# Kernel optimization log

Measured on AMD Instinct MI355X. Metric: run time of the kernel, lower is better.

## Reference

```python
import jax, jax.numpy as jnp
import numpy as np

HID = 2048      # hidden_size
NH = 32         # num_heads
QLR = 1536      # q_lora_rank
KVLR = 512      # kv_lora_rank
DR = 64         # qk_rope_head_dim
DN = 128        # qk_nope_head_dim
DV = 128        # v_head_dim
DQK = DN + DR   # 192
EPS = 1e-6
ROPE_BASE = 10000.0


def rms_norm(x, w):
    return x * jax.lax.rsqrt(jnp.mean(x * x, axis=-1, keepdims=True) + EPS) * w


def apply_rope(x, pos):
    # x: [B, S, H, d] (non-interleaved / rotate-half convention), pos: [S]
    d = x.shape[-1]
    inv_freq = 1.0 / (ROPE_BASE ** (jnp.arange(0, d, 2, dtype=jnp.float32) / d))
    freqs = pos[:, None].astype(jnp.float32) * inv_freq      # [S, d/2]
    cos = jnp.cos(freqs)[None, :, None, :]                   # [1, S, 1, d/2]
    sin = jnp.sin(freqs)[None, :, None, :]
    x1, x2 = x[..., : d // 2], x[..., d // 2:]
    return jnp.concatenate([x1 * cos - x2 * sin, x1 * sin + x2 * cos], axis=-1)


def setup_inputs() -> dict:
    key = jax.random.key(0)
    ks = jax.random.split(key, 8)
    s = 0.02
    return {
        "hidden_states": jax.random.normal(ks[0], (1, 2048, HID), jnp.float32),
        "q_a_w":    jax.random.normal(ks[1], (HID, QLR), jnp.float32) * s,
        "q_a_ln_w": jnp.ones((QLR,), jnp.float32),
        "q_b_w":    jax.random.normal(ks[2], (QLR, NH * DQK), jnp.float32) * s,
        "kv_a_w":   jax.random.normal(ks[3], (HID, KVLR + DR), jnp.float32) * s,
        "kv_a_ln_w": jnp.ones((KVLR,), jnp.float32),
        "kv_b_w":   jax.random.normal(ks[4], (KVLR, NH * (DN + DV)), jnp.float32) * s,
        "o_w":      jax.random.normal(ks[5], (NH * DV, HID), jnp.float32) * s,
    }


def reference(hidden_states, q_a_w, q_a_ln_w, q_b_w, kv_a_w, kv_a_ln_w, kv_b_w, o_w):
    B, S, _ = hidden_states.shape
    # low-rank Q: down-proj -> RMSNorm -> up-proj
    q = rms_norm(hidden_states @ q_a_w, q_a_ln_w) @ q_b_w       # [B,S,NH*DQK]
    q = q.reshape(B, S, NH, DQK)
    q_pass, q_rot = q[..., :DN], q[..., DN:]
    # compressed KV + shared rope key
    ckv = hidden_states @ kv_a_w                                # [B,S,KVLR+DR]
    c_kv, k_rot = ckv[..., :KVLR], ckv[..., KVLR:]
    kv = rms_norm(c_kv, kv_a_ln_w) @ kv_b_w                     # [B,S,NH*(DN+DV)]
    kv = kv.reshape(B, S, NH, DN + DV)
    k_pass, v = kv[..., :DN], kv[..., DN:]
    # RoPE
    pos = jnp.arange(S)
    q_rot = apply_rope(q_rot, pos)                              # [B,S,NH,DR]
    k_rot = apply_rope(k_rot[:, :, None, :], pos)[:, :, 0, :]   # [B,S,DR] (shared head)
    # causal attention, scale = qk_head_dim**-0.5
    scale = DQK ** -0.5
    scores = (jnp.einsum('bqhd,bkhd->bhqk', q_pass, k_pass)
              + jnp.einsum('bqhd,bkd->bhqk', q_rot, k_rot)) * scale
    causal = jnp.tril(jnp.ones((S, S), dtype=bool))
    scores = jnp.where(causal[None, None], scores, jnp.finfo(scores.dtype).min)
    p = jax.nn.softmax(scores, axis=-1)
    out = jnp.einsum('bhqk,bkhd->bqhd', p, v).reshape(B, S, NH * DV)
    return out @ o_w
```

## Files before the change

kernel.cpp:

```cpp
#include <hip/hip_runtime.h>


typedef __bf16 bf16x8 __attribute__((ext_vector_type(8)));
typedef float  f32x4  __attribute__((ext_vector_type(4)));
typedef unsigned u32x4 __attribute__((ext_vector_type(4)));

#define GLOAD16(g, l)                                                          \
  __builtin_amdgcn_global_load_lds(                                            \
      (const __attribute__((address_space(1))) unsigned int*)(g),              \
      (__attribute__((address_space(3))) unsigned int*)(l), 16, 0, 0)

__device__ __forceinline__ unsigned short f2b(float f) {
  unsigned u = __builtin_bit_cast(unsigned, f);
  u += 0x7fffu + ((u >> 16) & 1u);
  return (unsigned short)(u >> 16);
}

__device__ __forceinline__ unsigned cvtpk(float lo, float hi) {
  unsigned r;
  asm("v_cvt_pk_bf16_f32 %0, %1, %2" : "=v"(r) : "v"(lo), "v"(hi));
  return r;
}

__device__ __forceinline__ void tc_body(const float* __restrict__ src,
                                        unsigned short* __restrict__ dst,
                                        int R, int C, int bx, int by,
                                        int tx, int ty) {
  __shared__ float t[32][33];
  int r0 = bx * 32, c0 = by * 32;
#pragma unroll
  for (int j = 0; j < 4; j++) {
    int c = c0 + tx;
    t[ty + j * 8][tx] = (c < C) ? src[(size_t)(r0 + ty + j * 8) * C + c] : 0.f;
  }
  __syncthreads();
#pragma unroll
  for (int j = 0; j < 4; j++)
    dst[(size_t)(c0 + ty + j * 8) * R + r0 + tx] = f2b(t[tx][ty + j * 8]);
}

__global__ __launch_bounds__(256) void prep(
    const float* __restrict__ hs, unsigned short* __restrict__ hs_b,
    const float* __restrict__ qaw, const float* __restrict__ kvaw,
    unsigned short* __restrict__ wcat,
    const float* __restrict__ qbw, unsigned short* __restrict__ qbT,
    const float* __restrict__ kvbw, unsigned short* __restrict__ kvbT,
    const float* __restrict__ ow, unsigned short* __restrict__ owT) {
  int b = blockIdx.x;
// ... 146 lines not shown
    for (int n = 0; n < 4; n++) {
      int row = wn * 64 + n * 16 + lr;
      b[n] = *(const bf16x8*)(Bs + row * 32 + ((lh ^ swzr) * 8));
    }
#pragma unroll
    for (int m = 0; m < 4; m++)
#pragma unroll
      for (int n = 0; n < 4; n++)
        acc[m][n] = __builtin_amdgcn_mfma_f32_16x16x32_bf16(a[m], b[n], acc[m][n], 0, 0, 0);
    __syncthreads();
  }
#pragma unroll
  for (int m = 0; m < 4; m++)
#pragma unroll
    for (int n = 0; n < 4; n++)
#pragma unroll
      for (int r = 0; r < 4; r++) {
        int row = m0 + wm * 64 + m * 16 + lh * 4 + r;
        int col = n0 + wn * 64 + n * 16 + lr;
        C[(size_t)row * N + col] = acc[m][n][r];
      }
}

__global__ __launch_bounds__(512) void gemm256m(
    const unsigned short* __restrict__ Aq, const unsigned short* __restrict__ Bq,
    unsigned short* __restrict__ Qb,
    const unsigned short* __restrict__ Akv, const unsigned short* __restrict__ Bkv,
    unsigned short* __restrict__ Kb, unsigned short* __restrict__ Vt) {
  __shared__ unsigned short lds[2][2][16384];
  const int tid = threadIdx.x;
  const int w = tid >> 6, lane = tid & 63;
  const int lr = lane & 15, lh = lane >> 4;
  const int wr = w >> 2, wc = w & 3;
  const int blk = blockIdx.x;
  const bool isq = blk < 192;
  const int bx = isq ? (blk % 24) : ((blk - 192) & 31);
  const int by = isq ? (blk / 24) : ((blk - 192) >> 5);
  const int K  = isq ? 1536 : 512;
  const unsigned short* A  = isq ? Aq : Akv;
  const unsigned short* Bt = isq ? Bq : Bkv;
  const int m0 = by * 256, n0 = bx * 256;

  int soff[2];
#pragma unroll
  for (int j = 0; j < 2; j++) {
    int c = j * 512 + tid;
    int row = c >> 3, p = c & 7;
    soff[j] = row * K + (p ^ (row & 7)) * 8;
  }
  const unsigned short* Abase = A + (size_t)m0 * K;
  const unsigned short* Bbase = Bt + (size_t)n0 * K;
  const int rswz = lr & 7;

#define STAGEOP(op, Base, kt, buf)                                             \
  {                                                                            \
    _Pragma("unroll") for (int hh = 0; hh < 2; hh++)                           \
    _Pragma("unroll") for (int j = 0; j < 2; j++)                              \
      GLOAD16(Base + (size_t)(hh * 128) * K + soff[j] + (kt) * 64,             \
              &lds[buf][op][(hh * 1024 + j * 512 + w * 64) * 8]);              \
  }
#define READA(mh, buf)                                                         \
  {                                                                            \
    _Pragma("unroll") for (int mi = 0; mi < 4; mi++)                           \
    _Pragma("unroll") for (int ks = 0; ks < 2; ks++)                           \
      af[mi][ks] = *(const bf16x8*)&lds[buf][0][                               \
          (wr * 128 + ((mh) * 4 + mi) * 16 + lr) * 64 +                        \
          (((ks * 4 + lh) ^ rswz) * 8)];                                       \
// ... 137 lines not shown
  const int lin = blockIdx.x;
  const int sid = (lin & 7) * 32 + (lin >> 3);
  const int s = sid >> 6, rem = sid & 63;
  const int m0 = (rem >> 3) * 256, n0 = (rem & 7) * 256;
  const int Kst = 4096;
  const int koff = s * 1024;

  int soff[2];
#pragma unroll
  for (int j = 0; j < 2; j++) {
    int c = j * 512 + tid;
    int row = c >> 3, p = c & 7;
    soff[j] = row * Kst + (p ^ (row & 7)) * 8;
  }
  const unsigned short* Abase = A + (size_t)m0 * Kst + koff;
  const unsigned short* Bbase = Bt + (size_t)n0 * Kst + koff;
  const int rswz = lr & 7;

#define STAGEOP(op, Base, kt, buf)                                             \
  {                                                                            \
    _Pragma("unroll") for (int hh = 0; hh < 2; hh++)                           \
    _Pragma("unroll") for (int j = 0; j < 2; j++)                              \
      GLOAD16(Base + (size_t)(hh * 128) * Kst + soff[j] + (kt) * 64,           \
              &lds[buf][op][(hh * 1024 + j * 512 + w * 64) * 8]);              \
  }
#define READA(mh, buf)                                                         \
  {                                                                            \
    _Pragma("unroll") for (int mi = 0; mi < 4; mi++)                           \
    _Pragma("unroll") for (int ks = 0; ks < 2; ks++)                           \
      af[mi][ks] = *(const bf16x8*)&lds[buf][0][                               \
          (wr * 128 + ((mh) * 4 + mi) * 16 + lr) * 64 +                        \
          (((ks * 4 + lh) ^ rswz) * 8)];                                       \
  }
#define READB(n, buf)                                                          \
  {                                                                            \
    _Pragma("unroll") for (int ks = 0; ks < 2; ks++)                           \
      bfr[n][ks] = *(const bf16x8*)&lds[buf][1][                               \
          (wc * 64 + (n) * 16 + lr) * 64 + (((ks * 4 + lh) ^ rswz) * 8)];      \
  }
#define MFMAQ(mh, nh)                                                          \
  {                                                                            \
    __builtin_amdgcn_s_setprio(1);                                             \
    _Pragma("unroll") for (int mi = 0; mi < 4; mi++)                           \
    _Pragma("unroll") for (int ni = 0; ni < 2; ni++)                           \
    _Pragma("unroll") for (int ks = 0; ks < 2; ks++)                           \
      acc[(mh) * 4 + mi][(nh) * 2 + ni] =                                      \
          __builtin_amdgcn_mfma_f32_16x16x32_bf16(                             \
              af[mi][ks], bfr[(nh) * 2 + ni][ks],                              \
              acc[(mh) * 4 + mi][(nh) * 2 + ni], 0, 0, 0);                     \
    __builtin_amdgcn_s_setprio(0);                                             \
  }

  f32x4 acc[8][4];
  const f32x4 z = {0.f, 0.f, 0.f, 0.f};
#pragma unroll
  for (int i = 0; i < 8; i++)
#pragma unroll
    for (int j = 0; j < 4; j++) acc[i][j] = z;

  STAGEOP(0, Abase, 0, 0);
  STAGEOP(1, Bbase, 0, 0);
  asm volatile("s_waitcnt vmcnt(0)" ::: "memory");
  __builtin_amdgcn_s_barrier();

  const int KT = 16;
  for (int kt = 0; kt < KT; ++kt) {
    const int buf = kt & 1;
// ... 9 lines not shown
    if (more) STAGEOP(1, Bbase, kt + 1, buf ^ 1);
    __builtin_amdgcn_s_barrier();
    MFMAQ(0, 1);
    __builtin_amdgcn_s_barrier();
    READA(1, buf);
    __builtin_amdgcn_s_barrier();
    MFMAQ(1, 1);
    __builtin_amdgcn_s_barrier();
    MFMAQ(1, 0);
    if (more) asm volatile("s_waitcnt vmcnt(0)" ::: "memory");
    __builtin_amdgcn_s_barrier();
  }
#undef STAGEOP
#undef READA
#undef READB
#undef MFMAQ

  float* C = Cp + (size_t)s * 2048 * 2048;
#pragma unroll
  for (int m = 0; m < 8; m++)
#pragma unroll
    for (int n = 0; n < 4; n++)
#pragma unroll
      for (int r = 0; r < 4; r++) {
        int row = m0 + wr * 128 + m * 16 + lh * 4 + r;
        int col = n0 + wc * 64 + n * 16 + lr;
        C[(size_t)row * 2048 + col] = acc[m][n][r];
      }
}

__global__ __launch_bounds__(512) void attn(const unsigned short* __restrict__ Qb,
                                            const unsigned short* __restrict__ Kb,
                                            const unsigned short* __restrict__ Vt,
                                            unsigned short* __restrict__ O) {
  __shared__ unsigned short Kl[2][12288];
  __shared__ unsigned short Vl[2][8192];
  const int tid = threadIdx.x;
  const int w = tid >> 6, lane = tid & 63;
  const int lr = lane & 15, lh = lane >> 4;
  const int b = blockIdx.x;
  const int x = b & 7, k = b >> 3;
  const int h = x + 8 * (k >> 4);
  const int ii = k & 15;
  int qi = (ii & 1) ? (15 - 2 * (ii >> 1)) : (2 * (ii >> 1));
  if (k & 32) qi = 15 - qi;
  const int q0 = qi * 128;
  const int qw = q0 + w * 16;
  const int qv = qw + lr;

  bf16x8 qf[6];
#pragma unroll
  for (int c = 0; c < 6; c++)
    qf[c] = *(const bf16x8*)(Qb + (size_t)(qw + lr) * 6144 + h * 192 + c * 32 + lh * 8);

  const unsigned short* Kbase = Kb + h * 192;
  const unsigned short* Vbase = Vt + (size_t)h * 128 * 2048;
  size_t ka[3];
#pragma unroll
  for (int j = 0; j < 3; j++) {
    int c = tid + j * 512;
    int r = c / 24, p = c - r * 24;
    ka[j] = (size_t)r * 6144 + (p ^ (r & 7)) * 8;
  }
  size_t va[2];
#pragma unroll
  for (int j = 0; j < 2; j++) {
    int c = tid + j * 512;
    int d = c >> 3, p = c & 7;
    va[j] = (size_t)d * 2048 + (p ^ (d & 7)) * 8;
  }

#define STAGE(T0, B)                                                           \
  {                                                                            \
    _Pragma("unroll") for (int j = 0; j < 3; j++)                              \
        GLOAD16(Kbase + (size_t)(T0) * 6144 + ka[j], &Kl[B][(tid + j * 512) * 8]); \
    _Pragma("unroll") for (int j = 0; j < 2; j++)                              \
        GLOAD16(Vbase + va[j] + (T0), &Vl[B][(tid + j * 512) * 8]);            \
  }

  f32x4 acc[8];
  const f32x4 z = {0.f, 0.f, 0.f, 0.f};
#pragma unroll
  for (int n = 0; n < 8; n++) acc[n] = z;
  float mrow = -1e30f, lrow = 0.f;
  const int swz = (lr & 7) * 8;
  const int cv0 = ((lh ^ (lr & 7)) * 8);
  const int cv1 = (((4 + lh) ^ (lr & 7)) * 8);
  const int sA = lr + 32 * (lh & 1), sB = sA + 16;

  const int nt = (q0 + 128) >> 6;
  STAGE(0, 0);
  __syncthreads();
  for (int it = 0; it < nt; ++it) {
    const int t0 = it << 6;
    const int cur = it & 1;
    if (it + 1 < nt) STAGE(t0 + 64, cur ^ 1);
    if (t0 <= qw + 15) {
      f32x4 s0 = z, s1 = z, s2 = z, s3 = z;
      __builtin_amdgcn_s_setprio(1);
#pragma unroll
      for (int c = 0; c < 6; c++) {
        int col = ((c * 4 + lh) * 8) ^ swz;
        bf16x8 k0 = *(const bf16x8*)(&Kl[cur][(lr)      * 192 + col]);
        bf16x8 k1 = *(const bf16x8*)(&Kl[cur][(16 + lr) * 192 + col]);
        bf16x8 k2 = *(const bf16x8*)(&Kl[cur][(32 + lr) * 192 + col]);
        bf16x8 k3 = *(const bf16x8*)(&Kl[cur][(48 + lr) * 192 + col]);
        s0 = __builtin_amdgcn_mfma_f32_16x16x32_bf16(k0, qf[c], s0, 0, 0, 0);
        s1 = __builtin_amdgcn_mfma_f32_16x16x32_bf16(k1, qf[c], s1, 0, 0, 0);
        s2 = __builtin_amdgcn_mfma_f32_16x16x32_bf16(k2, qf[c], s2, 0, 0, 0);
        s3 = __builtin_amdgcn_mfma_f32_16x16x32_bf16(k3, qf[c], s3, 0, 0, 0);
      }
      __builtin_amdgcn_s_setprio(0);
      const int tb = t0 + lh * 4;
      if (t0 + 63 > qw) {
#pragma unroll
        for (int r = 0; r < 4; r++) {
          s0[r] = (tb + r > qv)      ? -1e30f : s0[r];
          s1[r] = (tb + 16 + r > qv) ? -1e30f : s1[r];
          s2[r] = (tb + 32 + r > qv) ? -1e30f : s2[r];
          s3[r] = (tb + 48 + r > qv) ? -1e30f : s3[r];
        }
      }
      float mx = -1e30f;
#pragma unroll
      for (int r = 0; r < 4; r++)
        mx = fmaxf(mx, fmaxf(fmaxf(s0[r], s1[r]), fmaxf(s2[r], s3[r])));
      mx = fmaxf(mx, __shfl_xor(mx, 16, 64));
      mx = fmaxf(mx, __shfl_xor(mx, 32, 64));
      float ro = 1.f;
      bool resc = (mx - mrow) > 11.5f;
      if (resc) { ro = exp2f(mrow - mx); mrow = mx; }
      float p0[4], p1[4], p2[4], p3[4], ls = 0.f;
#pragma unroll
      for (int r = 0; r < 4; r++) {
        p0[r] = exp2f(s0[r] - mrow);
        p1[r] = exp2f(s1[r] - mrow);
        p2[r] = exp2f(s2[r] - mrow);
        p3[r] = exp2f(s3[r] - mrow);
        ls += (p0[r] + p1[r]) + (p2[r] + p3[r]);
      }
      lrow = lrow * ro + ls;
      if (__any(resc)) {
        float rs[4];
#pragma unroll
        for (int r = 0; r < 4; r++) rs[r] = __shfl(ro, lh * 4 + r, 16);
#pragma unroll
        for (int n = 0; n < 8; n++)
#pragma unroll
          for (int r = 0; r < 4; r++) acc[n][r] *= rs[r];
      }
      unsigned k0p = cvtpk(p0[0], p0[1]), k1p = cvtpk(p0[2], p0[3]);
      unsigned k2p = cvtpk(p1[0], p1[1]), k3p = cvtpk(p1[2], p1[3]);
      unsigned k4p = cvtpk(p2[0], p2[1]), k5p = cvtpk(p2[2], p2[3]);
      unsigned k6p = cvtpk(p3[0], p3[1]), k7p = cvtpk(p3[2], p3[3]);
      u32x4 w0, w1;
      {
        unsigned A0 = __shfl(k0p, sA, 64), A1 = __shfl(k1p, sA, 64);
        unsigned B0 = __shfl(k0p, sB, 64), B1 = __shfl(k1p, sB, 64);
        unsigned C0 = __shfl(k2p, sA, 64), C1 = __shfl(k3p, sA, 64);
        unsigned D0 = __shfl(k2p, sB, 64), D1 = __shfl(k3p, sB, 64);
        w0[0] = (lh < 2) ? A0 : C0;
        w0[1] = (lh < 2) ? A1 : C1;
        w0[2] = (lh < 2) ? B0 : D0;
        w0[3] = (lh < 2) ? B1 : D1;
      }
      {
        unsigned A0 = __shfl(k4p, sA, 64), A1 = __shfl(k5p, sA, 64);
        unsigned B0 = __shfl(k4p, sB, 64), B1 = __shfl(k5p, sB, 64);
        unsigned C0 = __shfl(k6p, sA, 64), C1 = __shfl(k7p, sA, 64);
        unsigned D0 = __shfl(k6p, sB, 64), D1 = __shfl(k7p, sB, 64);
        w1[0] = (lh < 2) ? A0 : C0;
        w1[1] = (lh < 2) ? A1 : C1;
        w1[2] = (lh < 2) ? B0 : D0;
        w1[3] = (lh < 2) ? B1 : D1;
      }
      bf16x8 pa0 = __builtin_bit_cast(bf16x8, w0);
      bf16x8 pa1 = __builtin_bit_cast(bf16x8, w1);
      __builtin_amdgcn_s_setprio(1);
#pragma unroll
      for (int n = 0; n < 8; n++) {
        bf16x8 vb0 = *(const bf16x8*)(&Vl[cur][(n * 16 + lr) * 64 + cv0]);
        bf16x8 vb1 = *(const bf16x8*)(&Vl[cur][(n * 16 + lr) * 64 + cv1]);
        acc[n] = __builtin_amdgcn_mfma_f32_16x16x32_bf16(pa0, vb0, acc[n], 0, 0, 0);
        acc[n] = __builtin_amdgcn_mfma_f32_16x16x32_bf16(pa1, vb1, acc[n], 0, 0, 0);
      }
      __builtin_amdgcn_s_setprio(0);
    }
    __syncthreads();
  }
#undef STAGE
  lrow += __shfl_xor(lrow, 16, 64);
  lrow += __shfl_xor(lrow, 32, 64);
  float invL = 1.f / lrow;
  float inv[4];
#pragma unroll
  for (int r = 0; r < 4; r++) inv[r] = __shfl(invL, lh * 4 + r, 16);
#pragma unroll
  for (int n = 0; n < 8; n++)
#pragma unroll
    for (int r = 0; r < 4; r++) {
      int q = qw + lh * 4 + r;
      O[(size_t)q * 4096 + h * 128 + n * 16 + lr] = f2b(acc[n][r] * inv[r]);
    }
}

extern "C" void kernel_launch(void* const* d_in, const int* in_sizes, int n_in,
                              void* d_out, int out_size, void* d_ws, size_t ws_size,
                              hipStream_t stream) {
  const float* hs      = (const float*)d_in[0];
  const float* q_a_w   = (const float*)d_in[1];
  const float* q_a_ln  = (const float*)d_in[2];
  const float* q_b_w   = (const float*)d_in[3];
  const float* kv_a_w  = (const float*)d_in[4];
  const float* kv_a_ln = (const float*)d_in[5];
  const float* kv_b_w  = (const float*)d_in[6];
  const float* o_w     = (const float*)d_in[7];
  float* out = (float*)d_out;

  char* ws = (char*)d_ws;
  size_t off = 0;
  auto alloc = [&](size_t bytes) {
    void* p = ws + off;
    off += (bytes + 255) & ~(size_t)255;
    return p;
  };
  unsigned short* wcat    = (unsigned short*)alloc(2176UL * 2048 * 2);
  unsigned short* q_b_wT  = (unsigned short*)alloc(6144UL * 1536 * 2);
  unsigned short* kv_b_wT = (unsigned short*)alloc(8192UL * 512 * 2);
  unsigned short* o_wT    = (unsigned short*)alloc(2048UL * 4096 * 2);
  unsigned short* hs_b    = (unsigned short*)alloc(2048UL * 2048 * 2);
  unsigned short* q_a_n   = (unsigned short*)alloc(2048UL * 1536 * 2);
  unsigned short* Qb      = (unsigned short*)alloc(2048UL * 6144 * 2);
  unsigned short* ckv_n   = (unsigned short*)alloc(2048UL * 512 * 2);
  unsigned short* Kb      = (unsigned short*)alloc(2048UL * 6144 * 2);
  unsigned short* Vt      = (unsigned short*)alloc(32UL * 128 * 2048 * 2);
  float*          OutP    = (float*)Qb;
  char* big = (char*)alloc(2UL * 2048 * 2176 * 4);
  float*          Craw0    = (float*)big;
  float*          Craw1    = (float*)(big + 2048UL * 2176 * 4);
  unsigned short* attn_out = (unsigned short*)big;
  (void)ws_size; (void)in_sizes; (void)n_in; (void)out_size;

  dim3 b256(256), b512(512);
  prep<<<29952, b256, 0, stream>>>(hs, hs_b, q_a_w, kv_a_w, wcat,
                                   q_b_w, q_b_wT, kv_b_w, kv_b_wT, o_w, o_wT);
  gemm_bt<<<544, b256, 0, stream>>>(hs_b, wcat, Craw0, 2048, 2176, 2048, 17, 272, 2);
  rms2<<<4096, b256, 0, stream>>>(Craw0, Craw1, q_a_ln, kv_a_ln, q_a_n, ckv_n, Kb);
  gemm256m<<<448, b512, 0, stream>>>(q_a_n, q_b_wT, Qb, ckv_n, kv_b_wT, Kb, Vt);
  attn<<<512, b512, 0, stream>>>(Qb, Kb, Vt, attn_out);
  gemm256_op<<<256, b512, 0, stream>>>(attn_out, o_wT, OutP);
  addout<<<4096, b256, 0, stream>>>((const float4*)OutP, (float4*)out);
}
```

Before: 287.2 us.

## Split attention KV range by parity into two partials and add combine kernel

Attention blocks now each handle a pair of complementary query tiles (qi and 15-qi) and only the even or odd 32-key tiles, writing unnormalized-style partial outputs plus (max, sum) stats. A new combine kernel merges the two parity partials with log-sum-exp weights. The aim is to balance causal work evenly across blocks and to use smaller LDS tiles for better occupancy. The cost is an extra kernel launch, extra partial-output memory traffic and bf16 rounding of partials. The GEMM block index is also remapped for a different workgroup-to-CU distribution.

Measured after the change: 313.3 us. 1.09x slower.

```diff
diff --git a/kernel.cpp b/kernel.cpp
--- a/kernel.cpp
+++ b/kernel.cpp
@@ -14,6 +14,10 @@
   unsigned u = __builtin_bit_cast(unsigned, f);
   u += 0x7fffu + ((u >> 16) & 1u);
   return (unsigned short)(u >> 16);
+}
+
+__device__ __forceinline__ float b2f(unsigned short u) {
+  return __builtin_bit_cast(float, (unsigned)u << 16);
 }
 
 __device__ __forceinline__ unsigned cvtpk(float lo, float hi) {
@@ -226,7 +230,8 @@
   const int w = tid >> 6, lane = tid & 63;
   const int lr = lane & 15, lh = lane >> 4;
   const int wr = w >> 2, wc = w & 3;
-  const int blk = blockIdx.x;
+  const int lin = blockIdx.x;
+  const int blk = (lin & 7) * 56 + (lin >> 3);
   const bool isq = blk < 192;
   const int bx = isq ? (blk % 24) : ((blk - 192) & 31);
   const int by = isq ? (blk / 24) : ((blk - 192) >> 5);
@@ -506,176 +511,194 @@
 __global__ __launch_bounds__(512) void attn(const unsigned short* __restrict__ Qb,
                                             const unsigned short* __restrict__ Kb,
                                             const unsigned short* __restrict__ Vt,
-                                            unsigned short* __restrict__ O) {
-  __shared__ unsigned short Kl[2][12288];
-  __shared__ unsigned short Vl[2][8192];
+                                            unsigned short* __restrict__ Po,
+                                            float2* __restrict__ Ml) {
+  __shared__ unsigned short Kl[2][6144];
+  __shared__ unsigned short Vl[2][4096];
   const int tid = threadIdx.x;
   const int w = tid >> 6, lane = tid & 63;
   const int lr = lane & 15, lh = lane >> 4;
   const int b = blockIdx.x;
-  const int x = b & 7, k = b >> 3;
-  const int h = x + 8 * (k >> 4);
-  const int ii = k & 15;
-  int qi = (ii & 1) ? (15 - 2 * (ii >> 1)) : (2 * (ii >> 1));
-  if (k & 32) qi = 15 - qi;
-  const int q0 = qi * 128;
-  const int qw = q0 + w * 16;
-  const int qv = qw + lr;
-
-  bf16x8 qf[6];
-#pragma unroll
-  for (int c = 0; c < 6; c++)
-    qf[c] = *(const bf16x8*)(Qb + (size_t)(qw + lr) * 6144 + h * 192 + c * 32 + lh * 8);
+  const int x = b & 7, r_ = b >> 3;
+  const int h = x + 8 * (r_ & 3);
+  const int p = r_ >> 2;
+  const int a = p >> 1, par = p & 1;
 
   const unsigned short* Kbase = Kb + h * 192;
   const unsigned short* Vbase = Vt + (size_t)h * 128 * 2048;
-  size_t ka[3];
-#pragma unroll
-  for (int j = 0; j < 3; j++) {
-    int c = tid + j * 512;
-    int r = c / 24, p = c - r * 24;
-    ka[j] = (size_t)r * 6144 + (p ^ (r & 7)) * 8;
-  }
-  size_t va[2];
-#pragma unroll
-  for (int j = 0; j < 2; j++) {
-    int c = tid + j * 512;
-    int d = c >> 3, p = c & 7;
-    va[j] = (size_t)d * 2048 + (p ^ (d & 7)) * 8;
+  size_t kga0, kga1 = 0;
+  {
+    int c = w * 64 + lane;
+    int rr = c / 24, pp = c - rr * 24;
+    kga0 = (size_t)rr * 6144 + (pp ^ (rr & 7)) * 8;
+  }
+  if (w < 4) {
+    int c = 512 + w * 64 + lane;
+    int rr = c / 24, pp = c - rr * 24;
+    kga1 = (size_t)rr * 6144 + (pp ^ (rr & 7)) * 8;
+  }
+  size_t vga;
+  {
+    int c = w * 64 + lane;
+    int d = c >> 2, pp = c & 3;
+    vga = (size_t)d * 2048 + (pp ^ ((d >> 1) & 3)) * 8;
   }
 
 #define STAGE(T0, B)                                                           \
   {                                                                            \
-    _Pragma("unroll") for (int j = 0; j < 3; j++)                              \
-        GLOAD16(Kbase + (size_t)(T0) * 6144 + ka[j], &Kl[B][(tid + j * 512) * 8]); \
-    _Pragma("unroll") for (int j = 0; j < 2; j++)                              \
-        GLOAD16(Vbase + va[j] + (T0), &Vl[B][(tid + j * 512) * 8]);            \
-  }
-
-  f32x4 acc[8];
+    GLOAD16(Kbase + (size_t)(T0) * 6144 + kga0, &Kl[B][w * 512]);              \
+    if (w < 4)                                                                 \
+      GLOAD16(Kbase + (size_t)(T0) * 6144 + kga1, &Kl[B][4096 + w * 512]);     \
+    GLOAD16(Vbase + vga + (T0), &Vl[B][w * 512]);                              \
+  }
+
+  const int swz = (lr & 7) * 8;
+  const int vsw = (lh ^ ((lr >> 1) & 3)) * 8;
+  const int sA = lr + 32 * (lh & 1), sB = sA + 16;
   const f32x4 z = {0.f, 0.f, 0.f, 0.f};
-#pragma unroll
-  for (int n = 0; n < 8; n++) acc[n] = z;
-  float mrow = -1e30f, lrow = 0.f;
-  const int swz = (lr & 7) * 8;
-  const int cv0 = ((lh ^ (lr & 7)) * 8);
-  const int cv1 = (((4 + lh) ^ (lr & 7)) * 8);
-  const int sA = lr + 32 * (lh & 1), sB = sA + 16;
-
-  const int nt = (q0 + 128) >> 6;
-  STAGE(0, 0);
-  __syncthreads();
-  for (int it = 0; it < nt; ++it) {
-    const int t0 = it << 6;
-    const int cur = it & 1;
-    if (it + 1 < nt) STAGE(t0 + 64, cur ^ 1);
-    if (t0 <= qw + 15) {
-      f32x4 s0 = z, s1 = z, s2 = z, s3 = z;
-      __builtin_amdgcn_s_setprio(1);
-#pragma unroll
-      for (int c = 0; c < 6; c++) {
-        int col = ((c * 4 + lh) * 8) ^ swz;
-        bf16x8 k0 = *(const bf16x8*)(&Kl[cur][(lr)      * 192 + col]);
-        bf16x8 k1 = *(const bf16x8*)(&Kl[cur][(16 + lr) * 192 + col]);
-        bf16x8 k2 = *(const bf16x8*)(&Kl[cur][(32 + lr) * 192 + col]);
-        bf16x8 k3 = *(const bf16x8*)(&Kl[cur][(48 + lr) * 192 + col]);
-        s0 = __builtin_amdgcn_mfma_f32_16x16x32_bf16(k0, qf[c], s0, 0, 0, 0);
-        s1 = __builtin_amdgcn_mfma_f32_16x16x32_bf16(k1, qf[c], s1, 0, 0, 0);
-        s2 = __builtin_amdgcn_mfma_f32_16x16x32_bf16(k2, qf[c], s2, 0, 0, 0);
-        s3 = __builtin_amdgcn_mfma_f32_16x16x32_bf16(k3, qf[c], s3, 0, 0, 0);
+
+  for (int job = 0; job < 2; ++job) {
+    const int qi = job ? (15 - a) : a;
+    const int q0 = qi << 7;
+    const int qw = q0 + w * 16;
+    const int qv = qw + lr;
+    const int cnt = 2 * (qi + 1);
+
+    bf16x8 qf[6];
+#pragma unroll
+    for (int cc = 0; cc < 6; cc++)
+      qf[cc] = *(const bf16x8*)(Qb + (size_t)(qw + lr) * 6144 + h * 192 + cc * 32 + lh * 8);
+
+    f32x4 acc[8];
+#pragma unroll
+    for (int n = 0; n < 8; n++) acc[n] = z;
+    float mrow = -1e30f, lrow = 0.f;
+
+    STAGE((size_t)(par) << 5, 0);
+    __syncthreads();
+    for (int k = 0; k < cnt; ++k) {
+      const int t0 = (par + 2 * k) << 5;
+      const int cur = k & 1;
+      if (k + 1 < cnt) STAGE((size_t)(par + 2 * (k + 1)) << 5, cur ^ 1);
+      if (t0 <= qw + 15) {
+        f32x4 s0 = z, s1 = z;
+        __builtin_amdgcn_s_setprio(1);
+#pragma unroll
+        for (int cc = 0; cc < 6; cc++) {
+          int col = ((cc * 4 + lh) * 8) ^ swz;
+          bf16x8 k0 = *(const bf16x8*)(&Kl[cur][lr * 192 + col]);
+          bf16x8 k1 = *(const bf16x8*)(&Kl[cur][(16 + lr) * 192 + col]);
+          s0 = __builtin_amdgcn_mfma_f32_16x16x32_bf16(k0, qf[cc], s0, 0, 0, 0);
+          s1 = __builtin_amdgcn_mfma_f32_16x16x32_bf16(k1, qf[cc], s1, 0, 0, 0);
+        }
+        __builtin_amdgcn_s_setprio(0);
+        const int tb = t0 + lh * 4;
+        if (t0 + 31 > qw) {
+#pragma unroll
+          for (int r = 0; r < 4; r++) {
+            s0[r] = (tb + r > qv)      ? -1e30f : s0[r];
+            s1[r] = (tb + 16 + r > qv) ? -1e30f : s1[r];
+          }
+        }
+        float mx = -1e30f;
+#pragma unroll
+        for (int r = 0; r < 4; r++)
+          mx = fmaxf(mx, fmaxf(s0[r], s1[r]));
+        mx = fmaxf(mx, __shfl_xor(mx, 16, 64));
+        mx = fmaxf(mx, __shfl_xor(mx, 32, 64));
+        float ro = 1.f;
+        bool resc = (mx - mrow) > 11.5f;
+        if (resc) { ro = exp2f(mrow - mx); mrow = mx; }
+        float p0[4], p1[4], ls = 0.f;
+#pragma unroll
+        for (int r = 0; r < 4; r++) {
+          p0[r] = exp2f(s0[r] - mrow);
+          p1[r] = exp2f(s1[r] - mrow);
+          ls += p0[r] + p1[r];
+        }
+        lrow = lrow * ro + ls;
+        if (__any(resc)) {
+          float rs[4];
+#pragma unroll
+          for (int r = 0; r < 4; r++) rs[r] = __shfl(ro, lh * 4 + r, 16);
+#pragma unroll
+          for (int n = 0; n < 8; n++)
+#pragma unroll
+            for (int r = 0; r < 4; r++) acc[n][r] *= rs[r];
+        }
+        unsigned pk0 = cvtpk(p0[0], p0[1]), pk1 = cvtpk(p0[2], p0[3]);
+        unsigned pk2 = cvtpk(p1[0], p1[1]), pk3 = cvtpk(p1[2], p1[3]);
+        unsigned A0 = __shfl(pk0, sA, 64), A1 = __shfl(pk1, sA, 64);
+        unsigned B0 = __shfl(pk0, sB, 64), B1 = __shfl(pk1, sB, 64);
+        unsigned C0 = __shfl(pk2, sA, 64), C1 = __shfl(pk3, sA, 64);
+        unsigned D0 = __shfl(pk2, sB, 64), D1 = __shfl(pk3, sB, 64);
+        u32x4 pw;
+        pw[0] = (lh < 2) ? A0 : C0;
+        pw[1] = (lh < 2) ? A1 : C1;
+        pw[2] = (lh < 2) ? B0 : D0;
+        pw[3] = (lh < 2) ? B1 : D1;
+        bf16x8 pa = __builtin_bit_cast(bf16x8, pw);
+        __builtin_amdgcn_s_setprio(1);
+#pragma unroll
+        for (int n = 0; n < 8; n++) {
+          bf16x8 vb = *(const bf16x8*)(&Vl[cur][(n * 16 + lr) * 32 + vsw]);
+          acc[n] = __builtin_amdgcn_mfma_f32_16x16x32_bf16(pa, vb, acc[n], 0, 0, 0);
+        }
+        __builtin_amdgcn_s_setprio(0);
       }
-      __builtin_amdgcn_s_setprio(0);
-      const int tb = t0 + lh * 4;
-      if (t0 + 63 > qw) {
-#pragma unroll
-        for (int r = 0; r < 4; r++) {
-          s0[r] = (tb + r > qv)      ? -1e30f : s0[r];
-          s1[r] = (tb + 16 + r > qv) ? -1e30f : s1[r];
-          s2[r] = (tb + 32 + r > qv) ? -1e30f : s2[r];
-          s3[r] = (tb + 48 + r > qv) ? -1e30f : s3[r];
-        }
+      __syncthreads();
+    }
+    lrow += __shfl_xor(lrow, 16, 64);
+    lrow += __shfl_xor(lrow, 32, 64);
+    float invL = (lrow > 0.f) ? (1.f / lrow) : 0.f;
+    float inv[4];
+#pragma unroll
+    for (int r = 0; r < 4; r++) inv[r] = __shfl(invL, lh * 4 + r, 16);
+    unsigned short* Pob = Po + (size_t)par * 8388608;
+#pragma unroll
+    for (int n = 0; n < 8; n++)
+#pragma unroll
+      for (int r = 0; r < 4; r++) {
+        int q = qw + lh * 4 + r;
+        Pob[(size_t)q * 4096 + h * 128 + n * 16 + lr] = f2b(acc[n][r] * inv[r]);
       }
-      float mx = -1e30f;
-#pragma unroll
-      for (int r = 0; r < 4; r++)
-        mx = fmaxf(mx, fmaxf(fmaxf(s0[r], s1[r]), fmaxf(s2[r], s3[r])));
-      mx = fmaxf(mx, __shfl_xor(mx, 16, 64));
-      mx = fmaxf(mx, __shfl_xor(mx, 32, 64));
-      float ro = 1.f;
-      bool resc = (mx - mrow) > 11.5f;
-      if (resc) { ro = exp2f(mrow - mx); mrow = mx; }
-      float p0[4], p1[4], p2[4], p3[4], ls = 0.f;
-#pragma unroll
-      for (int r = 0; r < 4; r++) {
-        p0[r] = exp2f(s0[r] - mrow);
-        p1[r] = exp2f(s1[r] - mrow);
-        p2[r] = exp2f(s2[r] - mrow);
-        p3[r] = exp2f(s3[r] - mrow);
-        ls += (p0[r] + p1[r]) + (p2[r] + p3[r]);
-      }
-      lrow = lrow * ro + ls;
-      if (__any(resc)) {
-        float rs[4];
-#pragma unroll
-        for (int r = 0; r < 4; r++) rs[r] = __shfl(ro, lh * 4 + r, 16);
-#pragma unroll
-        for (int n = 0; n < 8; n++)
-#pragma unroll
-          for (int r = 0; r < 4; r++) acc[n][r] *= rs[r];
-      }
-      unsigned k0p = cvtpk(p0[0], p0[1]), k1p = cvtpk(p0[2], p0[3]);
-      unsigned k2p = cvtpk(p1[0], p1[1]), k3p = cvtpk(p1[2], p1[3]);
-      unsigned k4p = cvtpk(p2[0], p2[1]), k5p = cvtpk(p2[2], p2[3]);
-      unsigned k6p = cvtpk(p3[0], p3[1]), k7p = cvtpk(p3[2], p3[3]);
-      u32x4 w0, w1;
-      {
-        unsigned A0 = __shfl(k0p, sA, 64), A1 = __shfl(k1p, sA, 64);
-        unsigned B0 = __shfl(k0p, sB, 64), B1 = __shfl(k1p, sB, 64);
-        unsigned C0 = __shfl(k2p, sA, 64), C1 = __shfl(k3p, sA, 64);
-        unsigned D0 = __shfl(k2p, sB, 64), D1 = __shfl(k3p, sB, 64);
-        w0[0] = (lh < 2) ? A0 : C0;
-        w0[1] = (lh < 2) ? A1 : C1;
-        w0[2] = (lh < 2) ? B0 : D0;
-        w0[3] = (lh < 2) ? B1 : D1;
-      }
-      {
-        unsigned A0 = __shfl(k4p, sA, 64), A1 = __shfl(k5p, sA, 64);
-        unsigned B0 = __shfl(k4p, sB, 64), B1 = __shfl(k5p, sB, 64);
-        unsigned C0 = __shfl(k6p, sA, 64), C1 = __shfl(k7p, sA, 64);
-        unsigned D0 = __shfl(k6p, sB, 64), D1 = __shfl(k7p, sB, 64);
-        w1[0] = (lh < 2) ? A0 : C0;
-        w1[1] = (lh < 2) ? A1 : C1;
-        w1[2] = (lh < 2) ? B0 : D0;
-        w1[3] = (lh < 2) ? B1 : D1;
-      }
-      bf16x8 pa0 = __builtin_bit_cast(bf16x8, w0);
-      bf16x8 pa1 = __builtin_bit_cast(bf16x8, w1);
-      __builtin_amdgcn_s_setprio(1);
-#pragma unroll
-      for (int n = 0; n < 8; n++) {
-        bf16x8 vb0 = *(const bf16x8*)(&Vl[cur][(n * 16 + lr) * 64 + cv0]);
-        bf16x8 vb1 = *(const bf16x8*)(&Vl[cur][(n * 16 + lr) * 64 + cv1]);
-        acc[n] = __builtin_amdgcn_mfma_f32_16x16x32_bf16(pa0, vb0, acc[n], 0, 0, 0);
-        acc[n] = __builtin_amdgcn_mfma_f32_16x16x32_bf16(pa1, vb1, acc[n], 0, 0, 0);
-      }
-      __builtin_amdgcn_s_setprio(0);
-    }
-    __syncthreads();
+    if (lh == 0) {
+      float2 ml; ml.x = mrow; ml.y = lrow;
+      Ml[(size_t)par * 65536 + h * 2048 + qw + lr] = ml;
+    }
   }
 #undef STAGE
-  lrow += __shfl_xor(lrow, 16, 64);
-  lrow += __shfl_xor(lrow, 32, 64);
-  float invL = 1.f / lrow;
-  float inv[4];
-#pragma unroll
-  for (int r = 0; r < 4; r++) inv[r] = __shfl(invL, lh * 4 + r, 16);
-#pragma unroll
-  for (int n = 0; n < 8; n++)
-#pragma unroll
-    for (int r = 0; r < 4; r++) {
-      int q = qw + lh * 4 + r;
-      O[(size_t)q * 4096 + h * 128 + n * 16 + lr] = f2b(acc[n][r] * inv[r]);
-    }
+}
+
+__global__ __launch_bounds__(256) void combine(const unsigned short* __restrict__ Po,
+                                               const float2* __restrict__ Ml,
+                                               unsigned short* __restrict__ Out) {
+  int gid = blockIdx.x * 256 + threadIdx.x;
+  int row = gid >> 4, seg = gid & 15;
+  int q = row >> 5, h = row & 31;
+  float2 ml0 = Ml[h * 2048 + q];
+  float2 ml1 = Ml[65536 + h * 2048 + q];
+  float M = fmaxf(ml0.x, ml1.x);
+  float w0 = ml0.y * exp2f(ml0.x - M);
+  float w1 = ml1.y * exp2f(ml1.x - M);
+  float inv = 1.f / (w0 + w1);
+  w0 *= inv; w1 *= inv;
+  size_t off = (size_t)q * 4096 + h * 128 + seg * 8;
+  ushort4 a0 = *(const ushort4*)(Po + off);
+  ushort4 a1 = *(const ushort4*)(Po + off + 4);
+  ushort4 b0 = *(const ushort4*)(Po + 8388608 + off);
+  ushort4 b1 = *(const ushort4*)(Po + 8388608 + off + 4);
+  ushort4 o0, o1;
+  o0.x = f2b(w0 * b2f(a0.x) + w1 * b2f(b0.x));
+  o0.y = f2b(w0 * b2f(a0.y) + w1 * b2f(b0.y));
+  o0.z = f2b(w0 * b2f(a0.z) + w1 * b2f(b0.z));
+  o0.w = f2b(w0 * b2f(a0.w) + w1 * b2f(b0.w));
+  o1.x = f2b(w0 * b2f(a1.x) + w1 * b2f(b1.x));
+  o1.y = f2b(w0 * b2f(a1.y) + w1 * b2f(b1.y));
+  o1.z = f2b(w0 * b2f(a1.z) + w1 * b2f(b1.z));
+  o1.w = f2b(w0 * b2f(a1.w) + w1 * b2f(b1.w));
+  *(ushort4*)(Out + off) = o0;
+  *(ushort4*)(Out + off + 4) = o1;
 }
 
 extern "C" void kernel_launch(void* const* d_in, const int* in_sizes, int n_in,
@@ -712,7 +735,9 @@
   char* big = (char*)alloc(2UL * 2048 * 2176 * 4);
   float*          Craw0    = (float*)big;
   float*          Craw1    = (float*)(big + 2048UL * 2176 * 4);
-  unsigned short* attn_out = (unsigned short*)big;
+  unsigned short* Po       = (unsigned short*)big;
+  float2*         Ml       = (float2*)alloc(2UL * 32 * 2048 * 8);
+  unsigned short* attn_out = (unsigned short*)alloc(2048UL * 4096 * 2);
   (void)ws_size; (void)in_sizes; (void)n_in; (void)out_size;
 
   dim3 b256(256), b512(512);
@@ -721,7 +746,8 @@
   gemm_bt<<<544, b256, 0, stream>>>(hs_b, wcat, Craw0, 2048, 2176, 2048, 17, 272, 2);
   rms2<<<4096, b256, 0, stream>>>(Craw0, Craw1, q_a_ln, kv_a_ln, q_a_n, ckv_n, Kb);
   gemm256m<<<448, b512, 0, stream>>>(q_a_n, q_b_wT, Qb, ckv_n, kv_b_wT, Kb, Vt);
-  attn<<<512, b512, 0, stream>>>(Qb, Kb, Vt, attn_out);
+  attn<<<512, b512, 0, stream>>>(Qb, Kb, Vt, Po, Ml);
+  combine<<<4096, b256, 0, stream>>>(Po, Ml, attn_out);
   gemm256_op<<<256, b512, 0, stream>>>(attn_out, o_wT, OutP);
   addout<<<4096, b256, 0, stream>>>((const float4*)OutP, (float4*)out);
 }
```

## Split attention KV range by tile parity and merge partials in combine kernel

Applied to the files above, without the earlier changes.

Each attention block now handles one head, one KV parity (even or odd 64-key tiles), and two paired query tiles (a and 15-a). This balances causal work across blocks, which previously varied with query-tile position. Each half writes normalized bf16 partial outputs plus the row max and sum. A new combine kernel merges the two partials with log-sum-exp weights. The cost is an extra launch, extra global traffic for the partials, and extra bf16 rounding of the intermediate results.

After: 299.7 us. +4.3%, slower.

```diff
diff --git a/kernel.cpp b/kernel.cpp
--- a/kernel.cpp
+++ b/kernel.cpp
@@ -14,6 +14,10 @@
   unsigned u = __builtin_bit_cast(unsigned, f);
   u += 0x7fffu + ((u >> 16) & 1u);
   return (unsigned short)(u >> 16);
+}
+
+__device__ __forceinline__ float b2f(unsigned short u) {
+  return __builtin_bit_cast(float, (unsigned)u << 16);
 }
 
 __device__ __forceinline__ unsigned cvtpk(float lo, float hi) {
@@ -430,7 +434,7 @@
           (wr * 128 + ((mh) * 4 + mi) * 16 + lr) * 64 +                        \
           (((ks * 4 + lh) ^ rswz) * 8)];                                       \
   }
-#define READB(n, buf)                                                          \
+#define READB(n, buf)                                                         \
   {                                                                            \
     _Pragma("unroll") for (int ks = 0; ks < 2; ks++)                           \
       bfr[n][ks] = *(const bf16x8*)&lds[buf][1][                               \
@@ -506,26 +510,18 @@
 __global__ __launch_bounds__(512) void attn(const unsigned short* __restrict__ Qb,
                                             const unsigned short* __restrict__ Kb,
                                             const unsigned short* __restrict__ Vt,
-                                            unsigned short* __restrict__ O) {
+                                            unsigned short* __restrict__ Po,
+                                            float2* __restrict__ Ml) {
   __shared__ unsigned short Kl[2][12288];
   __shared__ unsigned short Vl[2][8192];
   const int tid = threadIdx.x;
   const int w = tid >> 6, lane = tid & 63;
   const int lr = lane & 15, lh = lane >> 4;
   const int b = blockIdx.x;
-  const int x = b & 7, k = b >> 3;
-  const int h = x + 8 * (k >> 4);
-  const int ii = k & 15;
-  int qi = (ii & 1) ? (15 - 2 * (ii >> 1)) : (2 * (ii >> 1));
-  if (k & 32) qi = 15 - qi;
-  const int q0 = qi * 128;
-  const int qw = q0 + w * 16;
-  const int qv = qw + lr;
-
-  bf16x8 qf[6];
-#pragma unroll
-  for (int c = 0; c < 6; c++)
-    qf[c] = *(const bf16x8*)(Qb + (size_t)(qw + lr) * 6144 + h * 192 + c * 32 + lh * 8);
+  const int x = b & 7, r_ = b >> 3;
+  const int h = x + 8 * (r_ & 3);
+  const int p = r_ >> 2;
+  const int a = p >> 1, par = p & 1;
 
   const unsigned short* Kbase = Kb + h * 192;
   const unsigned short* Vbase = Vt + (size_t)h * 128 * 2048;
@@ -533,15 +529,15 @@
 #pragma unroll
   for (int j = 0; j < 3; j++) {
     int c = tid + j * 512;
-    int r = c / 24, p = c - r * 24;
-    ka[j] = (size_t)r * 6144 + (p ^ (r & 7)) * 8;
+    int rr = c / 24, pp = c - rr * 24;
+    ka[j] = (size_t)rr * 6144 + (pp ^ (rr & 7)) * 8;
   }
   size_t va[2];
 #pragma unroll
   for (int j = 0; j < 2; j++) {
     int c = tid + j * 512;
-    int d = c >> 3, p = c & 7;
-    va[j] = (size_t)d * 2048 + (p ^ (d & 7)) * 8;
+    int d = c >> 3, pp = c & 7;
+    va[j] = (size_t)d * 2048 + (pp ^ (d & 7)) * 8;
   }
 
 #define STAGE(T0, B)                                                           \
@@ -552,130 +548,179 @@
         GLOAD16(Vbase + va[j] + (T0), &Vl[B][(tid + j * 512) * 8]);            \
   }
 
-  f32x4 acc[8];
-  const f32x4 z = {0.f, 0.f, 0.f, 0.f};
-#pragma unroll
-  for (int n = 0; n < 8; n++) acc[n] = z;
-  float mrow = -1e30f, lrow = 0.f;
   const int swz = (lr & 7) * 8;
   const int cv0 = ((lh ^ (lr & 7)) * 8);
   const int cv1 = (((4 + lh) ^ (lr & 7)) * 8);
   const int sA = lr + 32 * (lh & 1), sB = sA + 16;
-
-  const int nt = (q0 + 128) >> 6;
-  STAGE(0, 0);
-  __syncthreads();
-  for (int it = 0; it < nt; ++it) {
-    const int t0 = it << 6;
-    const int cur = it & 1;
-    if (it + 1 < nt) STAGE(t0 + 64, cur ^ 1);
-    if (t0 <= qw + 15) {
-      f32x4 s0 = z, s1 = z, s2 = z, s3 = z;
-      __builtin_amdgcn_s_setprio(1);
-#pragma unroll
-      for (int c = 0; c < 6; c++) {
-        int col = ((c * 4 + lh) * 8) ^ swz;
-        bf16x8 k0 = *(const bf16x8*)(&Kl[cur][(lr)      * 192 + col]);
-        bf16x8 k1 = *(const bf16x8*)(&Kl[cur][(16 + lr) * 192 + col]);
-        bf16x8 k2 = *(const bf16x8*)(&Kl[cur][(32 + lr) * 192 + col]);
-        bf16x8 k3 = *(const bf16x8*)(&Kl[cur][(48 + lr) * 192 + col]);
-        s0 = __builtin_amdgcn_mfma_f32_16x16x32_bf16(k0, qf[c], s0, 0, 0, 0);
-        s1 = __builtin_amdgcn_mfma_f32_16x16x32_bf16(k1, qf[c], s1, 0, 0, 0);
-        s2 = __builtin_amdgcn_mfma_f32_16x16x32_bf16(k2, qf[c], s2, 0, 0, 0);
-        s3 = __builtin_amdgcn_mfma_f32_16x16x32_bf16(k3, qf[c], s3, 0, 0, 0);
+  const f32x4 z = {0.f, 0.f, 0.f, 0.f};
+
+  for (int job = 0; job < 2; ++job) {
+    const int qi = job ? (15 - a) : a;
+    const int q0 = qi << 7;
+    const int qw = q0 + w * 16;
+    const int qv = qw + lr;
+    const int cnt = qi + 1;
+
+    bf16x8 qf[6];
+#pragma unroll
+    for (int cc = 0; cc < 6; cc++)
+      qf[cc] = *(const bf16x8*)(Qb + (size_t)(qw + lr) * 6144 + h * 192 + cc * 32 + lh * 8);
+
+    f32x4 acc[8];
+#pragma unroll
+    for (int n = 0; n < 8; n++) acc[n] = z;
+    float mrow = -1e30f, lrow = 0.f;
+
+    STAGE((size_t)par << 6, 0);
+    __syncthreads();
+    for (int k = 0; k < cnt; ++k) {
+      const int t0 = (par + 2 * k) << 6;
+      const int cur = k & 1;
+      if (k + 1 < cnt) STAGE((size_t)(par + 2 * (k + 1)) << 6, cur ^ 1);
+      if (t0 <= qw + 15) {
+        f32x4 s0 = z, s1 = z, s2 = z, s3 = z;
+        __builtin_amdgcn_s_setprio(1);
+#pragma unroll
+        for (int cc = 0; cc < 6; cc++) {
+          int col = ((cc * 4 + lh) * 8) ^ swz;
+          bf16x8 k0 = *(const bf16x8*)(&Kl[cur][(lr)      * 192 + col]);
+          bf16x8 k1 = *(const bf16x8*)(&Kl[cur][(16 + lr) * 192 + col]);
+          bf16x8 k2 = *(const bf16x8*)(&Kl[cur][(32 + lr) * 192 + col]);
+          bf16x8 k3 = *(const bf16x8*)(&Kl[cur][(48 + lr) * 192 + col]);
+          s0 = __builtin_amdgcn_mfma_f32_16x16x32_bf16(k0, qf[cc], s0, 0, 0, 0);
+          s1 = __builtin_amdgcn_mfma_f32_16x16x32_bf16(k1, qf[cc], s1, 0, 0, 0);
+          s2 = __builtin_amdgcn_mfma_f32_16x16x32_bf16(k2, qf[cc], s2, 0, 0, 0);
+          s3 = __builtin_amdgcn_mfma_f32_16x16x32_bf16(k3, qf[cc], s3, 0, 0, 0);
+        }
+        __builtin_amdgcn_s_setprio(0);
+        const int tb = t0 + lh * 4;
+        if (t0 + 63 > qw) {
+#pragma unroll
+          for (int r = 0; r < 4; r++) {
+            s0[r] = (tb + r > qv)      ? -1e30f : s0[r];
+            s1[r] = (tb + 16 + r > qv) ? -1e30f : s1[r];
+            s2[r] = (tb + 32 + r > qv) ? -1e30f : s2[r];
+            s3[r] = (tb + 48 + r > qv) ? -1e30f : s3[r];
+          }
+        }
+        float mx = -1e30f;
+#pragma unroll
+        for (int r = 0; r < 4; r++)
+          mx = fmaxf(mx, fmaxf(fmaxf(s0[r], s1[r]), fmaxf(s2[r], s3[r])));
+        mx = fmaxf(mx, __shfl_xor(mx, 16, 64));
+        mx = fmaxf(mx, __shfl_xor(mx, 32, 64));
+        float ro = 1.f;
+        bool resc = (mx - mrow) > 11.5f;
+        if (resc) { ro = exp2f(mrow - mx); mrow = mx; }
+        float p0[4], p1[4], p2[4], p3[4], ls = 0.f;
+#pragma unroll
+        for (int r = 0; r < 4; r++) {
+          p0[r] = exp2f(s0[r] - mrow);
+          p1[r] = exp2f(s1[r] - mrow);
+          p2[r] = exp2f(s2[r] - mrow);
+          p3[r] = exp2f(s3[r] - mrow);
+          ls += (p0[r] + p1[r]) + (p2[r] + p3[r]);
+        }
+        lrow = lrow * ro + ls;
+        if (__any(resc)) {
+          float rs[4];
+#pragma unroll
+          for (int r = 0; r < 4; r++) rs[r] = __shfl(ro, lh * 4 + r, 16);
+#pragma unroll
+          for (int n = 0; n < 8; n++)
+#pragma unroll
+            for (int r = 0; r < 4; r++) acc[n][r] *= rs[r];
+        }
+        unsigned k0p = cvtpk(p0[0], p0[1]), k1p = cvtpk(p0[2], p0[3]);
+        unsigned k2p = cvtpk(p1[0], p1[1]), k3p = cvtpk(p1[2], p1[3]);
+        unsigned k4p = cvtpk(p2[0], p2[1]), k5p = cvtpk(p2[2], p2[3]);
+        unsigned k6p = cvtpk(p3[0], p3[1]), k7p = cvtpk(p3[2], p3[3]);
+        u32x4 w0, w1;
+        {
+          unsigned A0 = __shfl(k0p, sA, 64), A1 = __shfl(k1p, sA, 64);
+          unsigned B0 = __shfl(k0p, sB, 64), B1 = __shfl(k1p, sB, 64);
+          unsigned C0 = __shfl(k2p, sA, 64), C1 = __shfl(k3p, sA, 64);
+          unsigned D0 = __shfl(k2p, sB, 64), D1 = __shfl(k3p, sB, 64);
+          w0[0] = (lh < 2) ? A0 : C0;
+          w0[1] = (lh < 2) ? A1 : C1;
+          w0[2] = (lh < 2) ? B0 : D0;
+          w0[3] = (lh < 2) ? B1 : D1;
+        }
+        {
+          unsigned A0 = __shfl(k4p, sA, 64), A1 = __shfl(k5p, sA, 64);
+          unsigned B0 = __shfl(k4p, sB, 64), B1 = __shfl(k5p, sB, 64);
+          unsigned C0 = __shfl(k6p, sA, 64), C1 = __shfl(k7p, sA, 64);
+          unsigned D0 = __shfl(k6p, sB, 64), D1 = __shfl(k7p, sB, 64);
+          w1[0] = (lh < 2) ? A0 : C0;
+          w1[1] = (lh < 2) ? A1 : C1;
+          w1[2] = (lh < 2) ? B0 : D0;
+          w1[3] = (lh < 2) ? B1 : D1;
+        }
+        bf16x8 pa0 = __builtin_bit_cast(bf16x8, w0);
+        bf16x8 pa1 = __builtin_bit_cast(bf16x8, w1);
+        __builtin_amdgcn_s_setprio(1);
+#pragma unroll
+        for (int n = 0; n < 8; n++) {
+          bf16x8 vb0 = *(const bf16x8*)(&Vl[cur][(n * 16 + lr) * 64 + cv0]);
+          bf16x8 vb1 = *(const bf16x8*)(&Vl[cur][(n * 16 + lr) * 64 + cv1]);
+          acc[n] = __builtin_amdgcn_mfma_f32_16x16x32_bf16(pa0, vb0, acc[n], 0, 0, 0);
+          acc[n] = __builtin_amdgcn_mfma_f32_16x16x32_bf16(pa1, vb1, acc[n], 0, 0, 0);
+        }
+        __builtin_amdgcn_s_setprio(0);
       }
-      __builtin_amdgcn_s_setprio(0);
-      const int tb = t0 + lh * 4;
-      if (t0 + 63 > qw) {
-#pragma unroll
-        for (int r = 0; r < 4; r++) {
-          s0[r] = (tb + r > qv)      ? -1e30f : s0[r];
-          s1[r] = (tb + 16 + r > qv) ? -1e30f : s1[r];
-          s2[r] = (tb + 32 + r > qv) ? -1e30f : s2[r];
-          s3[r] = (tb + 48 + r > qv) ? -1e30f : s3[r];
-        }
+      __syncthreads();
+    }
+    lrow += __shfl_xor(lrow, 16, 64);
+    lrow += __shfl_xor(lrow, 32, 64);
+    float invL = (lrow > 0.f) ? (1.f / lrow) : 0.f;
+    float inv[4];
+#pragma unroll
+    for (int r = 0; r < 4; r++) inv[r] = __shfl(invL, lh * 4 + r, 16);
+    unsigned short* Pob = Po + (size_t)par * 8388608;
+#pragma unroll
+    for (int n = 0; n < 8; n++)
+#pragma unroll
+      for (int r = 0; r < 4; r++) {
+        int q = qw + lh * 4 + r;
+        Pob[(size_t)q * 4096 + h * 128 + n * 16 + lr] = f2b(acc[n][r] * inv[r]);
       }
-      float mx = -1e30f;
-#pragma unroll
-      for (int r = 0; r < 4; r++)
-        mx = fmaxf(mx, fmaxf(fmaxf(s0[r], s1[r]), fmaxf(s2[r], s3[r])));
-      mx = fmaxf(mx, __shfl_xor(mx, 16, 64));
-      mx = fmaxf(mx, __shfl_xor(mx, 32, 64));
-      float ro = 1.f;
-      bool resc = (mx - mrow) > 11.5f;
-      if (resc) { ro = exp2f(mrow - mx); mrow = mx; }
-      float p0[4], p1[4], p2[4], p3[4], ls = 0.f;
-#pragma unroll
-      for (int r = 0; r < 4; r++) {
-        p0[r] = exp2f(s0[r] - mrow);
-        p1[r] = exp2f(s1[r] - mrow);
-        p2[r] = exp2f(s2[r] - mrow);
-        p3[r] = exp2f(s3[r] - mrow);
-        ls += (p0[r] + p1[r]) + (p2[r] + p3[r]);
-      }
-      lrow = lrow * ro + ls;
-      if (__any(resc)) {
-        float rs[4];
-#pragma unroll
-        for (int r = 0; r < 4; r++) rs[r] = __shfl(ro, lh * 4 + r, 16);
-#pragma unroll
-        for (int n = 0; n < 8; n++)
-#pragma unroll
-          for (int r = 0; r < 4; r++) acc[n][r] *= rs[r];
-      }
-      unsigned k0p = cvtpk(p0[0], p0[1]), k1p = cvtpk(p0[2], p0[3]);
-      unsigned k2p = cvtpk(p1[0], p1[1]), k3p = cvtpk(p1[2], p1[3]);
-      unsigned k4p = cvtpk(p2[0], p2[1]), k5p = cvtpk(p2[2], p2[3]);
-      unsigned k6p = cvtpk(p3[0], p3[1]), k7p = cvtpk(p3[2], p3[3]);
-      u32x4 w0, w1;
-      {
-        unsigned A0 = __shfl(k0p, sA, 64), A1 = __shfl(k1p, sA, 64);
-        unsigned B0 = __shfl(k0p, sB, 64), B1 = __shfl(k1p, sB, 64);
-        unsigned C0 = __shfl(k2p, sA, 64), C1 = __shfl(k3p, sA, 64);
-        unsigned D0 = __shfl(k2p, sB, 64), D1 = __shfl(k3p, sB, 64);
-        w0[0] = (lh < 2) ? A0 : C0;
-        w0[1] = (lh < 2) ? A1 : C1;
-        w0[2] = (lh < 2) ? B0 : D0;
-        w0[3] = (lh < 2) ? B1 : D1;
-      }
-      {
-        unsigned A0 = __shfl(k4p, sA, 64), A1 = __shfl(k5p, sA, 64);
-        unsigned B0 = __shfl(k4p, sB, 64), B1 = __shfl(k5p, sB, 64);
-        unsigned C0 = __shfl(k6p, sA, 64), C1 = __shfl(k7p, sA, 64);
-        unsigned D0 = __shfl(k6p, sB, 64), D1 = __shfl(k7p, sB, 64);
-        w1[0] = (lh < 2) ? A0 : C0;
-        w1[1] = (lh < 2) ? A1 : C1;
-        w1[2] = (lh < 2) ? B0 : D0;
-        w1[3] = (lh < 2) ? B1 : D1;
-      }
-      bf16x8 pa0 = __builtin_bit_cast(bf16x8, w0);
-      bf16x8 pa1 = __builtin_bit_cast(bf16x8, w1);
-      __builtin_amdgcn_s_setprio(1);
-#pragma unroll
-      for (int n = 0; n < 8; n++) {
-        bf16x8 vb0 = *(const bf16x8*)(&Vl[cur][(n * 16 + lr) * 64 + cv0]);
-        bf16x8 vb1 = *(const bf16x8*)(&Vl[cur][(n * 16 + lr) * 64 + cv1]);
-        acc[n] = __builtin_amdgcn_mfma_f32_16x16x32_bf16(pa0, vb0, acc[n], 0, 0, 0);
-        acc[n] = __builtin_amdgcn_mfma_f32_16x16x32_bf16(pa1, vb1, acc[n], 0, 0, 0);
-      }
-      __builtin_amdgcn_s_setprio(0);
-    }
-    __syncthreads();
+    if (lh == 0) {
+      float2 ml; ml.x = mrow; ml.y = lrow;
+      Ml[(size_t)par * 65536 + h * 2048 + qw + lr] = ml;
+    }
   }
 #undef STAGE
-  lrow += __shfl_xor(lrow, 16, 64);
-  lrow += __shfl_xor(lrow, 32, 64);
-  float invL = 1.f / lrow;
-  float inv[4];
-#pragma unroll
-  for (int r = 0; r < 4; r++) inv[r] = __shfl(invL, lh * 4 + r, 16);
-#pragma unroll
-  for (int n = 0; n < 8; n++)
-#pragma unroll
-    for (int r = 0; r < 4; r++) {
-      int q = qw + lh * 4 + r;
-      O[(size_t)q * 4096 + h * 128 + n * 16 + lr] = f2b(acc[n][r] * inv[r]);
-    }
+}
+
+__global__ __launch_bounds__(256) void combine(const unsigned short* __restrict__ Po,
+                                               const float2* __restrict__ Ml,
+                                               unsigned short* __restrict__ Out) {
+  int gid = blockIdx.x * 256 + threadIdx.x;
+  int row = gid >> 4, seg = gid & 15;
+  int q = row >> 5, h = row & 31;
+  float2 ml0 = Ml[h * 2048 + q];
+  float2 ml1 = Ml[65536 + h * 2048 + q];
+  float M = fmaxf(ml0.x, ml1.x);
+  float w0 = ml0.y * exp2f(ml0.x - M);
+  float w1 = ml1.y * exp2f(ml1.x - M);
+  float inv = 1.f / (w0 + w1);
+  w0 *= inv; w1 *= inv;
+  size_t off = (size_t)q * 4096 + h * 128 + seg * 8;
+  ushort4 a0 = *(const ushort4*)(Po + off);
+  ushort4 a1 = *(const ushort4*)(Po + off + 4);
+  ushort4 b0 = *(const ushort4*)(Po + 8388608 + off);
+  ushort4 b1 = *(const ushort4*)(Po + 8388608 + off + 4);
+  ushort4 o0, o1;
+  o0.x = f2b(w0 * b2f(a0.x) + w1 * b2f(b0.x));
+  o0.y = f2b(w0 * b2f(a0.y) + w1 * b2f(b0.y));
+  o0.z = f2b(w0 * b2f(a0.z) + w1 * b2f(b0.z));
+  o0.w = f2b(w0 * b2f(a0.w) + w1 * b2f(b0.w));
+  o1.x = f2b(w0 * b2f(a1.x) + w1 * b2f(b1.x));
+  o1.y = f2b(w0 * b2f(a1.y) + w1 * b2f(b1.y));
+  o1.z = f2b(w0 * b2f(a1.z) + w1 * b2f(b1.z));
+  o1.w = f2b(w0 * b2f(a1.w) + w1 * b2f(b1.w));
+  *(ushort4*)(Out + off) = o0;
+  *(ushort4*)(Out + off + 4) = o1;
 }
 
 extern "C" void kernel_launch(void* const* d_in, const int* in_sizes, int n_in,
@@ -712,7 +757,9 @@
   char* big = (char*)alloc(2UL * 2048 * 2176 * 4);
   float*          Craw0    = (float*)big;
   float*          Craw1    = (float*)(big + 2048UL * 2176 * 4);
-  unsigned short* attn_out = (unsigned short*)big;
+  unsigned short* Po       = (unsigned short*)big;
+  float2*         Ml       = (float2*)alloc(2UL * 32 * 2048 * 8);
+  unsigned short* attn_out = (unsigned short*)alloc(2048UL * 4096 * 2);
   (void)ws_size; (void)in_sizes; (void)n_in; (void)out_size;
 
   dim3 b256(256), b512(512);
@@ -721,7 +768,8 @@
   gemm_bt<<<544, b256, 0, stream>>>(hs_b, wcat, Craw0, 2048, 2176, 2048, 17, 272, 2);
   rms2<<<4096, b256, 0, stream>>>(Craw0, Craw1, q_a_ln, kv_a_ln, q_a_n, ckv_n, Kb);
   gemm256m<<<448, b512, 0, stream>>>(q_a_n, q_b_wT, Qb, ckv_n, kv_b_wT, Kb, Vt);
-  attn<<<512, b512, 0, stream>>>(Qb, Kb, Vt, attn_out);
+  attn<<<512, b512, 0, stream>>>(Qb, Kb, Vt, Po, Ml);
+  combine<<<4096, b256, 0, stream>>>(Po, Ml, attn_out);
   gemm256_op<<<256, b512, 0, stream>>>(attn_out, o_wT, OutP);
   addout<<<4096, b256, 0, stream>>>((const float4*)OutP, (float4*)out);
 }
```
